# Kernel tuning notes

Measured on AMD Instinct MI355X. Metric: run time of the kernel, lower is better.

## Reference

```python
import jax, jax.numpy as jnp
import numpy as np

POOL = 2  # pool_size from init_kwargs


def setup_inputs() -> dict:
    key = jax.random.key(0)
    b, n = 8192, 64
    A = jax.random.normal(key, (b, n, n), dtype=jnp.float32)
    # SPD construction: A A^T / n + I  (well-conditioned, distinct eigvals a.s.)
    X = A @ jnp.swapaxes(A, -1, -2) / n + jnp.eye(n, dtype=jnp.float32)
    return {"X": X}


def _logm_spd(X):
    # matrix log of batched SPD via eigendecomposition (SPDTangentSpace)
    w, V = jnp.linalg.eigh(X)
    return (V * jnp.log(w)[..., None, :]) @ jnp.swapaxes(V, -1, -2)


def _expm_sym(H):
    # matrix exp of batched symmetric matrices (SPDUnTangentSpace)
    w, V = jnp.linalg.eigh(H)
    return (V * jnp.exp(w)[..., None, :]) @ jnp.swapaxes(V, -1, -2)


def reference(X):
    # log map to tangent space
    logX = _logm_spd(X)
    b, n, _ = logX.shape
    m = n // POOL
    # avg_pool2d(kernel=POOL, stride=POOL) over the (n, n) matrix dims
    pooled = logX.reshape(b, m, POOL, m, POOL).mean(axis=(2, 4))
    # pooling of a symmetric matrix with this block pattern stays symmetric;
    # symmetrize for numerical safety before eigh-based exp map
    pooled = 0.5 * (pooled + jnp.swapaxes(pooled, -1, -2))
    return _expm_sym(pooled)
```

## Files before the change

### kernel.cpp

```cpp
#include <hip/hip_runtime.h>

typedef __attribute__((ext_vector_type(8))) short short8;
typedef __attribute__((ext_vector_type(16))) float f32x16;

#define PL 8256
#define SLOT 16448
#define U0O 0
#define U1O SLOT
#define U2O (2 * SLOT)

__device__ __forceinline__ int swadr(int m, int kc) {
  return m * 128 + ((kc ^ (m & 7)) << 4);
}

__device__ __forceinline__ unsigned int cvtpk(float a, float b) {
  unsigned int r;
  asm("v_cvt_pk_bf16_f32 %0, %1, %2" : "=v"(r) : "v"(a), "v"(b));
  return r;
}

__device__ __forceinline__ float dppswap(float v) {
  return __int_as_float(
      __builtin_amdgcn_mov_dpp(__float_as_int(v), 0xB1, 0xF, 0xF, true));
}

__device__ __forceinline__ f32x16 zero16() {
  f32x16 z;
#pragma unroll
  for (int i = 0; i < 16; ++i) z[i] = 0.f;
  return z;
}

__device__ __forceinline__ void q16x16(f32x16& v) {
#pragma unroll
  for (int r = 0; r < 16; r += 2) {
    unsigned w = cvtpk(v[r], v[r + 1]);
    v[r] = __uint_as_float(w << 16);
    v[r + 1] = __uint_as_float(w & 0xFFFF0000u);
  }
}

__device__ __forceinline__ void store_hi8(char* dst, const float* v) {
  uint4 w = make_uint4(cvtpk(v[0], v[1]), cvtpk(v[2], v[3]),
                       cvtpk(v[4], v[5]), cvtpk(v[6], v[7]));
  *(uint4*)dst = w;
}

__device__ __forceinline__ void split_store8(char* dst, const float* v) {
  unsigned h[4], l[4];
#pragma unroll
  for (int j = 0; j < 4; ++j) {
    unsigned hw = cvtpk(v[2 * j], v[2 * j + 1]);
    float h0 = __uint_as_float(hw << 16);
    float h1 = __uint_as_float(hw & 0xFFFF0000u);
    l[j] = cvtpk(v[2 * j] - h0, v[2 * j + 1] - h1);
    h[j] = hw;
  }
  *(uint4*)dst = make_uint4(h[0], h[1], h[2], h[3]);
  *(uint4*)(dst + PL) = make_uint4(l[0], l[1], l[2], l[3]);
}

__device__ __forceinline__ void split_store4(char* dst, const float* v) {
  unsigned h0 = cvtpk(v[0], v[1]), h1 = cvtpk(v[2], v[3]);
  unsigned l0 = cvtpk(v[0] - __uint_as_float(h0 << 16),
                      v[1] - __uint_as_float(h0 & 0xFFFF0000u));
  unsigned l1 = cvtpk(v[2] - __uint_as_float(h1 << 16),
                      v[3] - __uint_as_float(h1 & 0xFFFF0000u));
  *(uint2*)dst = make_uint2(h0, h1);
  *(uint2*)(dst + PL) = make_uint2(l0, l1);
}

template <int NK, int OA, int OB>
__device__ __forceinline__ void mac1(f32x16& acc, char* const (&pA)[4],
                                     char* const (&pB)[4]) {
#pragma unroll
  for (int s = 0; s < NK; ++s) {
    short8 a = *(const short8*)(pA[s] + OA);
    short8 b = *(const short8*)(pB[s] + OB);
    acc = __builtin_amdgcn_mfma_f32_32x32x16_bf16(a, b, acc, 0, 0, 0);
  }
}

template <int NK, int OA, int OB>
__device__ __forceinline__ void mac2A(f32x16& acc, char* const (&pA)[4],
                                      char* const (&pB)[4]) {
#pragma unroll
  for (int s = 0; s < NK; ++s) {
    short8 ah = *(const short8*)(pA[s] + OA);
    short8 al = *(const short8*)(pA[s] + OA + PL);
    short8 b = *(const short8*)(pB[s] + OB);
    acc = __builtin_amdgcn_mfma_f32_32x32x16_bf16(ah, b, acc, 0, 0, 0);
    acc = __builtin_amdgcn_mfma_f32_32x32x16_bf16(al, b, acc, 0, 0, 0);
  }
}

template <int NK, int OA, int OB>
__device__ __forceinline__ void mac2B(f32x16& acc, char* const (&pA)[4],
                                      char* const (&pB)[4]) {
#pragma unroll
  for (int s = 0; s < NK; ++s) {
    short8 a = *(const short8*)(pA[s] + OA);
    short8 bh = *(const short8*)(pB[s] + OB);
    short8 bl = *(const short8*)(pB[s] + OB + PL);
    acc = __builtin_amdgcn_mfma_f32_32x32x16_bf16(a, bh, acc, 0, 0, 0);
    acc = __builtin_amdgcn_mfma_f32_32x32x16_bf16(a, bl, acc, 0, 0, 0);
  }
}

template <int NK, int OA, int OB>
__device__ __forceinline__ void mac3(f32x16& acc, char* const (&pA)[4],
                                     char* const (&pB)[4]) {
#pragma unroll
  for (int s = 0; s < NK; ++s) {
    short8 ah = *(const short8*)(pA[s] + OA);
    short8 al = *(const short8*)(pA[s] + OA + PL);
    short8 bh = *(const short8*)(pB[s] + OB);
    short8 bl = *(const short8*)(pB[s] + OB + PL);
    acc = __builtin_amdgcn_mfma_f32_32x32x16_bf16(ah, bh, acc, 0, 0, 0);
    acc = __builtin_amdgcn_mfma_f32_32x32x16_bf16(ah, bl, acc, 0, 0, 0);
    acc = __builtin_amdgcn_mfma_f32_32x32x16_bf16(al, bh, acc, 0, 0, 0);
  }
}

template <int OFF>
__device__ __forceinline__ void write_hi(char* lds, const int (&wo)[16], bool ev,
                                         const f32x16& vals) {
#pragma unroll
  for (int r = 0; r < 16; ++r) {
    float vn = dppswap(vals[r]);
    unsigned hw = cvtpk(vals[r], vn);
    if (ev) *(unsigned*)(lds + OFF + wo[r]) = hw;
  }
}

template <int OFF>
__device__ __forceinline__ void write_split(char* lds, const int (&wo)[16],
                                            bool ev, int pl, const f32x16& vals,
                                            int r0, int r1) {
#pragma unroll
  for (int r = 0; r < 16; ++r) {
    if (r < r0 || r >= r1) continue;
    float v = vals[r];
    float vn = dppswap(v);
    unsigned hw = cvtpk(v, vn);
    float lo = v - __uint_as_float(hw << 16);
    float lon = dppswap(lo);
    unsigned lw = cvtpk(lon, lo);
    *(unsigned*)(lds + OFF + pl + wo[r]) = ev ? hw : lw;
  }
}

__global__ void __launch_bounds__(256, 3)
spd_pool_kernel(const float* __restrict__ X, float* __restrict__ out) {
  __shared__ __align__(16) char lds[3 * SLOT];

  const int tid = threadIdx.x;
  const int lane = tid & 63;
  const int wv = tid >> 6;
  const int R = (wv >> 1) * 32;
  const int Cc = (wv & 1) * 32;
  const int half = lane >> 5;
  const int ln31 = lane & 31;
  const bool ev = (ln31 & 1) == 0;
  const int pl = ev ? 0 : PL;

  char* pA[4];
  char* pB[4];
#pragma unroll
  for (int s = 0; s < 4; ++s) {
    const int kc = 2 * s + half;
    pA[s] = lds + swadr(R + ln31, kc);
    pB[s] = lds + swadr(Cc + ln31, kc);
  }

  int wo[16];
  {
    const int col0 = Cc + (ln31 & ~1);
    const int cchunk = col0 >> 3, cbyte = (col0 & 7) * 2;
    const int rbase = R + 4 * half;
#pragma unroll
    for (int r = 0; r < 16; ++r) {
      const int m = rbase + (r & 3) + 8 * (r >> 2);
      wo[r] = m * 128 + ((cchunk ^ (m & 7)) << 4) + cbyte;
    }
  }

  f32x16 dmask;
#pragma unroll
  for (int r = 0; r < 16; ++r)
    dmask[r] = (R + (r & 3) + 8 * (r >> 2) + 4 * half == Cc + ln31) ? 1.f : 0.f;

  f32x16 mY, mZ;

  {
    const int em = tid >> 2;
    const int ekc = (tid & 3) * 2;
    const int ec0 = ekc * 8;
    const float ic1 = 1.0f / 6.6f;
    const float* Xg = X + (size_t)blockIdx.x * 4096 + em * 64 + ec0;
    const float4* xp = (const float4*)Xg;
    float4 a = xp[0], b = xp[1], c = xp[2], d = xp[3];
    float v[16] = {a.x * ic1, a.y * ic1, a.z * ic1, a.w * ic1,
                   b.x * ic1, b.y * ic1, b.z * ic1, b.w * ic1,
                   c.x * ic1, c.y * ic1, c.z * ic1, c.w * ic1,
                   d.x * ic1, d.y * ic1, d.z * ic1, d.w * ic1};
    float t[16];
#pragma unroll
    for (int i = 0; i < 16; ++i)
      t[i] = ((em == ec0 + i) ? 1.5f : 0.f) - 0.5f * v[i];
    split_store8(lds + swadr(em, ekc), v);
    split_store8(lds + swadr(em, ekc + 1), v + 8);
    store_hi8(lds + U1O + swadr(em, ekc), t);
    store_hi8(lds + U1O + swadr(em, ekc + 1), t + 8);
  }
  __syncthreads();
  mY = zero16();
  mac1<4, U0O, U1O>(mY, pA, pB);
  write_hi<U2O>(lds, wo, ev, mY);
  __syncthreads();
#pragma unroll 1
  for (int it = 0; it < 4; ++it) {
    f32x16 a;
#pragma unroll
    for (int r = 0; r < 16; ++r) a[r] = -3.f * dmask[r];
    mac1<4, U1O, U2O>(a, pA, pB);
    f32x16 tv;
#pragma unroll
    for (int r = 0; r < 16; ++r) tv[r] = -0.5f * a[r];
    write_hi<U2O + PL>(lds, wo, ev, tv);
    __syncthreads();
    mY = zero16();
    mac1<4, U2O, U2O + PL>(mY, pA, pB);
    mZ = zero16();
    mac1<4, U2O + PL, U1O>(mZ, pA, pB);
    __syncthreads();
    write_hi<U2O>(lds, wo, ev, mY);
    write_hi<U1O>(lds, wo, ev, mZ);
    __syncthreads();
  }
  mY = zero16();
  mac2A<4, U0O, U1O>(mY, pA, pB);
  write_split<U2O>(lds, wo, ev, pl, mY, 0, 16);
  __syncthreads();
  {
    f32x16 a;
#pragma unroll
    for (int r = 0; r < 16; ++r) a[r] = -dmask[r];
    mac2B<4, U1O, U2O>(a, pA, pB);
    f32x16 dv;
#pragma unroll
    for (int r = 0; r < 16; ++r) dv[r] = -0.5f * a[r];
    write_hi<U0O>(lds, wo, ev, dv);
  }
  __syncthreads();
  mac1<4, U2O, U0O>(mY, pA, pB);
  __syncthreads();
  write_split<U2O>(lds, wo, ev, pl, mY, 0, 16);
  {
    f32x16 t0v;
#pragma unroll
    for (int r = 0; r < 16; ++r) t0v[r] = 1.5f * dmask[r] - 0.5f * mY[r];
    write_hi<U1O>(lds, wo, ev, t0v);
  }
  __syncthreads();
  mY = zero16();
  mac1<4, U2O, U1O>(mY, pA, pB);
  write_hi<U0O>(lds, wo, ev, mY);
  __syncthreads();
#pragma unroll 1
  for (int it = 0; it < 2; ++it) {
    f32x16 a;
#pragma unroll
    for (int r = 0; r < 16; ++r) a[r] = -3.f * dmask[r];
    mac1<4, U1O, U0O>(a, pA, pB);
    f32x16 tv;
#pragma unroll
    for (int r = 0; r < 16; ++r) tv[r] = -0.5f * a[r];
    write_hi<U0O + PL>(lds, wo, ev, tv);
    __syncthreads();
    mY = zero16();
    mac1<4, U0O, U0O + PL>(mY, pA, pB);
    mZ = zero16();
    mac1<4, U0O + PL, U1O>(mZ, pA, pB);
    __syncthreads();
    write_hi<U0O>(lds, wo, ev, mY);
    write_hi<U1O>(lds, wo, ev, mZ);
    __syncthreads();
  }
  q16x16(mZ);
  mY = zero16();
  mac2A<4, U2O, U1O>(mY, pA, pB);
  write_split<U0O>(lds, wo, ev, pl, mY, 0, 16);
  __syncthreads();
  {
    f32x16 a;
#pragma unroll
    for (int r = 0; r < 16; ++r) a[r] = -dmask[r];
    mac2B<4, U1O, U0O>(a, pA, pB);
    f32x16 dv;
#pragma unroll
    for (int r = 0; r < 16; ++r) dv[r] = -0.5f * a[r];
    write_hi<U2O>(lds, wo, ev, dv);
  }
  __syncthreads();
  mac1<4, U0O, U2O>(mY, pA, pB);
  mac1<4, U2O, U1O>(mZ, pA, pB);
  __syncthreads();
  write_split<U0O>(lds, wo, ev, pl, mY, 0, 16);
  q16x16(mZ);
  write_hi<U1O>(lds, wo, ev, mZ);
  __syncthreads();
  {
    f32x16 a;
#pragma unroll
    for (int r = 0; r < 16; ++r) a[r] = -dmask[r];
    mac2B<4, U1O, U0O>(a, pA, pB);
    f32x16 dv;
#pragma unroll
    for (int r = 0; r < 16; ++r) dv[r] = -0.5f * a[r];
    write_hi<U2O>(lds, wo, ev, dv);
  }
  __syncthreads();
  mac1<4, U0O, U2O>(mY, pA, pB);
  mac1<4, U2O, U1O>(mZ, pA, pB);
  f32x16 sv;
  {
    const float ca = 0.80141224f;
    const float cb = 0.31194493f;
#pragma unroll
    for (int r = 0; r < 16; ++r) sv[r] = ca * mY[r] - cb * mZ[r];
  }
  __syncthreads();
  write_split<U0O>(lds, wo, ev, pl, sv, 0, 16);
  __syncthreads();
  {
    f32x16 s2 = zero16();
    mac3<4, U0O, U0O>(s2, pA, pB);
    const float A11 = -0.08948864f, A9 = 0.12152778f;
    f32x16 qv;
#pragma unroll
    for (int r = 0; r < 16; ++r) qv[r] = A11 * s2[r] + A9 * dmask[r];
    write_hi<U1O>(lds, wo, ev, s2);
    write_hi<U1O + PL>(lds, wo, ev, qv);
  }
  __syncthreads();
  {
    const float acoef[3] = {-0.17857143f, 0.3f, -0.66666667f};
#pragma unroll 1
    for (int j = 0; j < 3; ++j) {
      f32x16 a;
#pragma unroll
      for (int r = 0; r < 16; ++r) a[r] = acoef[j] * dmask[r];
      mac1<4, U1O + PL, U1O>(a, pA, pB);
      __syncthreads();
      write_hi<U1O + PL>(lds, wo, ev, a);
      __syncthreads();
    }
  }
  {
    f32x16 a;
#pragma unroll
    for (int r = 0; r < 16; ++r) a[r] = 4.f * dmask[r];
    mac1<4, U1O + PL, U1O>(a, pA, pB);
    __syncthreads();
    write_split<U2O>(lds, wo, ev, pl, a, 0, 16);
    __syncthreads();
  }
  {
    f32x16 mL = zero16();
    mac3<4, U0O, U2O>(mL, pA, pB);
    float* Lf = (float*)(lds + U1O);
#pragma unroll
    for (int r = 0; r < 16; ++r)
      Lf[(R + (r & 3) + 8 * (r >> 2) + 4 * half) * 64 + Cc + ln31] = mL[r];
  }
  __syncthreads();
  {
    const float d8 = 2.4801587e-5f, d7 = 1.9841270e-4f;
    const float* Lf = (const float*)(lds + U1O);
    int i = tid >> 3, ct = tid & 7, j4 = ct * 4;
    const float4* r0p = (const float4*)&Lf[(2 * i) * 64 + 8 * ct];
    const float4* r1p = (const float4*)&Lf[(2 * i + 1) * 64 + 8 * ct];
    float4 a0 = r0p[0], a1 = r0p[1], b0 = r1p[0], b1 = r1p[1];
    float p[4], q2v[4];
    p[0] = 0.125f * (a0.x + a0.y + b0.x + b0.y);
    p[1] = 0.125f * (a0.z + a0.w + b0.z + b0.w);
    p[2] = 0.125f * (a1.x + a1.y + b1.x + b1.y);
    p[3] = 0.125f * (a1.z + a1.w + b1.z + b1.w);
#pragma unroll
    for (int qq = 0; qq < 4; ++qq)
      q2v[qq] = d8 * p[qq] + ((i == j4 + qq) ? d7 : 0.f);
    int boff = swadr(i, ct >> 1) + (j4 & 7) * 2;
    split_store4(lds + boff, p);
    split_store4(lds + U2O + boff, q2v);
  }
  __syncthreads();
  char* pE[4];
#pragma unroll
  for (int s = 0; s < 4; ++s) pE[s] = lds + swadr(ln31, 2 * s + half);
  f32x16 dmask2;
#pragma unroll
  for (int r = 0; r < 16; ++r)
    dmask2[r] = ((r & 3) + 8 * (r >> 2) + 4 * half == ln31) ? 1.f : 0.f;
  int wo2[16];
  {
    const int col0 = ln31 & ~1;
    const int cchunk = col0 >> 3, cbyte = (col0 & 7) * 2;
    const int rbase = 4 * half;
#pragma unroll
    for (int r = 0; r < 16; ++r) {
      const int m = rbase + (r & 3) + 8 * (r >> 2);
      wo2[r] = m * 128 + ((cchunk ^ (m & 7)) << 4) + cbyte;
    }
  }
  {
    const float dcoef[7] = {1.f / 720.f, 1.f / 120.f, 1.f / 24.f,
                            1.f / 6.f,   0.5f,        1.f,       1.f};
#pragma unroll 1
    for (int j = 0; j < 7; ++j) {
      f32x16 acc;
#pragma unroll
      for (int r = 0; r < 16; ++r) acc[r] = dcoef[j] * dmask2[r];
      mac3<2, U2O, U0O>(acc, pE, pE);
      __syncthreads();
      write_split<U2O>(lds, wo2, ev, pl, acc, 4 * wv, 4 * wv + 4);
      __syncthreads();
    }
  }
  {
    f32x16 acc = zero16();
    mac3<2, U2O, U2O>(acc, pE, pE);
    float* og = out + (size_t)blockIdx.x * 1024;
#pragma unroll
    for (int r = 0; r < 16; ++r) {
      if (r < 4 * wv || r >= 4 * wv + 4) continue;
      int rl = (r & 3) + 8 * (r >> 2) + 4 * half;
      og[rl * 32 + ln31] = acc[r];
    }
  }
}

extern "C" void kernel_launch(void* const* d_in, const int* in_sizes, int n_in,
                              void* d_out, int out_size, void* d_ws, size_t ws_size,
                              hipStream_t stream) {
  const float* X = (const float*)d_in[0];
  float* out = (float*)d_out;
  const int batch = in_sizes[0] / 4096;
  spd_pool_kernel<<<batch, 256, 0, stream>>>(X, out);
}
```

Before: 541.5 us.

## Shrink LDS to five 8KB planes and pool in registers via DPP

Shared memory is reorganised from three padded 16448-byte slots into five unpadded 8KB planes (40KB instead of about 48KB), and launch bounds go from 3 to 4 blocks per CU so more workgroups can be resident. The 2x2 average pooling no longer stages the fp32 log matrix through LDS with an extra barrier. It is now computed in registers from the MFMA accumulator, using a DPP lane swap for the column pair. The results are split into bf16 hi/lo and written directly into the planes. The risks are register pressure under the tighter launch bound, more LDS bank conflicts now that the padding is gone, and many narrow 2-byte stores.

```diff
diff --git a/kernel.cpp b/kernel.cpp
--- a/kernel.cpp
+++ b/kernel.cpp
@@ -3,11 +3,12 @@
 typedef __attribute__((ext_vector_type(8))) short short8;
 typedef __attribute__((ext_vector_type(16))) float f32x16;
 
-#define PL 8256
-#define SLOT 16448
-#define U0O 0
-#define U1O SLOT
-#define U2O (2 * SLOT)
+#define PL 8192
+#define PP0 0
+#define PP1 8192
+#define PP2 16384
+#define PP3 24576
+#define PP4 32768
 
 __device__ __forceinline__ int swadr(int m, int kc) {
   return m * 128 + ((kc ^ (m & 7)) << 4);
@@ -18,19 +19,16 @@
   asm("v_cvt_pk_bf16_f32 %0, %1, %2" : "=v"(r) : "v"(a), "v"(b));
   return r;
 }
-
 __device__ __forceinline__ float dppswap(float v) {
   return __int_as_float(
       __builtin_amdgcn_mov_dpp(__float_as_int(v), 0xB1, 0xF, 0xF, true));
 }
-
 __device__ __forceinline__ f32x16 zero16() {
   f32x16 z;
 #pragma unroll
   for (int i = 0; i < 16; ++i) z[i] = 0.f;
   return z;
 }
-
 __device__ __forceinline__ void q16x16(f32x16& v) {
 #pragma unroll
   for (int r = 0; r < 16; r += 2) {
@@ -41,11 +39,9 @@
 }
 
 __device__ __forceinline__ void store_hi8(char* dst, const float* v) {
-  uint4 w = make_uint4(cvtpk(v[0], v[1]), cvtpk(v[2], v[3]),
-                       cvtpk(v[4], v[5]), cvtpk(v[6], v[7]));
-  *(uint4*)dst = w;
-}
-
+  *(uint4*)dst = make_uint4(cvtpk(v[0], v[1]), cvtpk(v[2], v[3]),
+                            cvtpk(v[4], v[5]), cvtpk(v[6], v[7]));
+}
 __device__ __forceinline__ void split_store8(char* dst, const float* v) {
   unsigned h[4], l[4];
 #pragma unroll
@@ -60,19 +56,9 @@
   *(uint4*)(dst + PL) = make_uint4(l[0], l[1], l[2], l[3]);
 }
 
-__device__ __forceinline__ void split_store4(char* dst, const float* v) {
-  unsigned h0 = cvtpk(v[0], v[1]), h1 = cvtpk(v[2], v[3]);
-  unsigned l0 = cvtpk(v[0] - __uint_as_float(h0 << 16),
-                      v[1] - __uint_as_float(h0 & 0xFFFF0000u));
-  unsigned l1 = cvtpk(v[2] - __uint_as_float(h1 << 16),
-                      v[3] - __uint_as_float(h1 & 0xFFFF0000u));
-  *(uint2*)dst = make_uint2(h0, h1);
-  *(uint2*)(dst + PL) = make_uint2(l0, l1);
-}
-
-template <int NK, int OA, int OB>
-__device__ __forceinline__ void mac1(f32x16& acc, char* const (&pA)[4],
-                                     char* const (&pB)[4]) {
+template <int NK, int OA, int OB, int N>
+__device__ __forceinline__ void mac1(f32x16& acc, char* const (&pA)[N],
+                                     char* const (&pB)[N]) {
 #pragma unroll
   for (int s = 0; s < NK; ++s) {
     short8 a = *(const short8*)(pA[s] + OA);
@@ -80,10 +66,9 @@
     acc = __builtin_amdgcn_mfma_f32_32x32x16_bf16(a, b, acc, 0, 0, 0);
   }
 }
-
-template <int NK, int OA, int OB>
-__device__ __forceinline__ void mac2A(f32x16& acc, char* const (&pA)[4],
-                                      char* const (&pB)[4]) {
+template <int NK, int OA, int OB, int N>
+__device__ __forceinline__ void mac2A(f32x16& acc, char* const (&pA)[N],
+                                      char* const (&pB)[N]) {
 #pragma unroll
   for (int s = 0; s < NK; ++s) {
     short8 ah = *(const short8*)(pA[s] + OA);
@@ -93,10 +78,9 @@
     acc = __builtin_amdgcn_mfma_f32_32x32x16_bf16(al, b, acc, 0, 0, 0);
   }
 }
-
-template <int NK, int OA, int OB>
-__device__ __forceinline__ void mac2B(f32x16& acc, char* const (&pA)[4],
-                                      char* const (&pB)[4]) {
+template <int NK, int OA, int OB, int N>
+__device__ __forceinline__ void mac2B(f32x16& acc, char* const (&pA)[N],
+                                      char* const (&pB)[N]) {
 #pragma unroll
   for (int s = 0; s < NK; ++s) {
     short8 a = *(const short8*)(pA[s] + OA);
@@ -106,10 +90,9 @@
     acc = __builtin_amdgcn_mfma_f32_32x32x16_bf16(a, bl, acc, 0, 0, 0);
   }
 }
-
-template <int NK, int OA, int OB>
-__device__ __forceinline__ void mac3(f32x16& acc, char* const (&pA)[4],
-                                     char* const (&pB)[4]) {
+template <int NK, int OA, int OB, int N>
+__device__ __forceinline__ void mac3(f32x16& acc, char* const (&pA)[N],
+                                     char* const (&pB)[N]) {
 #pragma unroll
   for (int s = 0; s < NK; ++s) {
     short8 ah = *(const short8*)(pA[s] + OA);
@@ -132,7 +115,6 @@
     if (ev) *(unsigned*)(lds + OFF + wo[r]) = hw;
   }
 }
-
 template <int OFF>
 __device__ __forceinline__ void write_split(char* lds, const int (&wo)[16],
                                             bool ev, int pl, const f32x16& vals,
@@ -150,9 +132,9 @@
   }
 }
 
-__global__ void __launch_bounds__(256, 3)
+__global__ void __launch_bounds__(256, 4)
 spd_pool_kernel(const float* __restrict__ X, float* __restrict__ out) {
-  __shared__ __align__(16) char lds[3 * SLOT];
+  __shared__ __align__(16) char lds[5 * 8192];
 
   const int tid = threadIdx.x;
   const int lane = tid & 63;
@@ -172,7 +154,6 @@
     pA[s] = lds + swadr(R + ln31, kc);
     pB[s] = lds + swadr(Cc + ln31, kc);
   }
-
   int wo[16];
   {
     const int col0 = Cc + (ln31 & ~1);
@@ -184,7 +165,6 @@
       wo[r] = m * 128 + ((cchunk ^ (m & 7)) << 4) + cbyte;
     }
   }
-
   f32x16 dmask;
 #pragma unroll
   for (int r = 0; r < 16; ++r)
@@ -208,121 +188,121 @@
 #pragma unroll
     for (int i = 0; i < 16; ++i)
       t[i] = ((em == ec0 + i) ? 1.5f : 0.f) - 0.5f * v[i];
-    split_store8(lds + swadr(em, ekc), v);
-    split_store8(lds + swadr(em, ekc + 1), v + 8);
-    store_hi8(lds + U1O + swadr(em, ekc), t);
-    store_hi8(lds + U1O + swadr(em, ekc + 1), t + 8);
+    split_store8(lds + PP0 + swadr(em, ekc), v);
+    split_store8(lds + PP0 + swadr(em, ekc + 1), v + 8);
+    store_hi8(lds + PP2 + swadr(em, ekc), t);
+    store_hi8(lds + PP2 + swadr(em, ekc + 1), t + 8);
   }
   __syncthreads();
   mY = zero16();
-  mac1<4, U0O, U1O>(mY, pA, pB);
-  write_hi<U2O>(lds, wo, ev, mY);
+  mac1<4, PP0, PP2>(mY, pA, pB);
+  write_hi<PP3>(lds, wo, ev, mY);
   __syncthreads();
 #pragma unroll 1
   for (int it = 0; it < 4; ++it) {
     f32x16 a;
 #pragma unroll
     for (int r = 0; r < 16; ++r) a[r] = -3.f * dmask[r];
-    mac1<4, U1O, U2O>(a, pA, pB);
+    mac1<4, PP2, PP3>(a, pA, pB);
     f32x16 tv;
 #pragma unroll
     for (int r = 0; r < 16; ++r) tv[r] = -0.5f * a[r];
-    write_hi<U2O + PL>(lds, wo, ev, tv);
+    write_hi<PP4>(lds, wo, ev, tv);
     __syncthreads();
     mY = zero16();
-    mac1<4, U2O, U2O + PL>(mY, pA, pB);
+    mac1<4, PP3, PP4>(mY, pA, pB);
     mZ = zero16();
-    mac1<4, U2O + PL, U1O>(mZ, pA, pB);
-    __syncthreads();
-    write_hi<U2O>(lds, wo, ev, mY);
-    write_hi<U1O>(lds, wo, ev, mZ);
+    mac1<4, PP4, PP2>(mZ, pA, pB);
+    __syncthreads();
+    write_hi<PP3>(lds, wo, ev, mY);
+    write_hi<PP2>(lds, wo, ev, mZ);
     __syncthreads();
   }
   mY = zero16();
-  mac2A<4, U0O, U1O>(mY, pA, pB);
-  write_split<U2O>(lds, wo, ev, pl, mY, 0, 16);
+  mac2A<4, PP0, PP2>(mY, pA, pB);
+  write_split<PP3>(lds, wo, ev, pl, mY, 0, 16);
   __syncthreads();
   {
     f32x16 a;
 #pragma unroll
     for (int r = 0; r < 16; ++r) a[r] = -dmask[r];
-    mac2B<4, U1O, U2O>(a, pA, pB);
+    mac2B<4, PP2, PP3>(a, pA, pB);
     f32x16 dv;
 #pragma unroll
     for (int r = 0; r < 16; ++r) dv[r] = -0.5f * a[r];
-    write_hi<U0O>(lds, wo, ev, dv);
-  }
-  __syncthreads();
-  mac1<4, U2O, U0O>(mY, pA, pB);
-  __syncthreads();
-  write_split<U2O>(lds, wo, ev, pl, mY, 0, 16);
+    write_hi<PP0>(lds, wo, ev, dv);
+  }
+  __syncthreads();
+  mac1<4, PP3, PP0>(mY, pA, pB);
+  __syncthreads();
+  write_split<PP3>(lds, wo, ev, pl, mY, 0, 16);
   {
     f32x16 t0v;
 #pragma unroll
     for (int r = 0; r < 16; ++r) t0v[r] = 1.5f * dmask[r] - 0.5f * mY[r];
-    write_hi<U1O>(lds, wo, ev, t0v);
+    write_hi<PP2>(lds, wo, ev, t0v);
   }
   __syncthreads();
   mY = zero16();
-  mac1<4, U2O, U1O>(mY, pA, pB);
-  write_hi<U0O>(lds, wo, ev, mY);
+  mac1<4, PP3, PP2>(mY, pA, pB);
+  write_hi<PP0>(lds, wo, ev, mY);
   __syncthreads();
 #pragma unroll 1
   for (int it = 0; it < 2; ++it) {
     f32x16 a;
 #pragma unroll
     for (int r = 0; r < 16; ++r) a[r] = -3.f * dmask[r];
-    mac1<4, U1O, U0O>(a, pA, pB);
+    mac1<4, PP2, PP0>(a, pA, pB);
     f32x16 tv;
 #pragma unroll
     for (int r = 0; r < 16; ++r) tv[r] = -0.5f * a[r];
-    write_hi<U0O + PL>(lds, wo, ev, tv);
+    write_hi<PP1>(lds, wo, ev, tv);
     __syncthreads();
     mY = zero16();
-    mac1<4, U0O, U0O + PL>(mY, pA, pB);
+    mac1<4, PP0, PP1>(mY, pA, pB);
     mZ = zero16();
-    mac1<4, U0O + PL, U1O>(mZ, pA, pB);
-    __syncthreads();
-    write_hi<U0O>(lds, wo, ev, mY);
-    write_hi<U1O>(lds, wo, ev, mZ);
+    mac1<4, PP1, PP2>(mZ, pA, pB);
+    __syncthreads();
+    write_hi<PP0>(lds, wo, ev, mY);
+    write_hi<PP2>(lds, wo, ev, mZ);
     __syncthreads();
   }
   q16x16(mZ);
   mY = zero16();
-  mac2A<4, U2O, U1O>(mY, pA, pB);
-  write_split<U0O>(lds, wo, ev, pl, mY, 0, 16);
+  mac2A<4, PP3, PP2>(mY, pA, pB);
+  write_split<PP0>(lds, wo, ev, pl, mY, 0, 16);
   __syncthreads();
   {
     f32x16 a;
 #pragma unroll
     for (int r = 0; r < 16; ++r) a[r] = -dmask[r];
-    mac2B<4, U1O, U0O>(a, pA, pB);
+    mac2B<4, PP2, PP0>(a, pA, pB);
     f32x16 dv;
 #pragma unroll
     for (int r = 0; r < 16; ++r) dv[r] = -0.5f * a[r];
-    write_hi<U2O>(lds, wo, ev, dv);
-  }
-  __syncthreads();
-  mac1<4, U0O, U2O>(mY, pA, pB);
-  mac1<4, U2O, U1O>(mZ, pA, pB);
-  __syncthreads();
-  write_split<U0O>(lds, wo, ev, pl, mY, 0, 16);
+    write_hi<PP3>(lds, wo, ev, dv);
+  }
+  __syncthreads();
+  mac1<4, PP0, PP3>(mY, pA, pB);
+  mac1<4, PP3, PP2>(mZ, pA, pB);
+  __syncthreads();
+  write_split<PP0>(lds, wo, ev, pl, mY, 0, 16);
   q16x16(mZ);
-  write_hi<U1O>(lds, wo, ev, mZ);
+  write_hi<PP2>(lds, wo, ev, mZ);
   __syncthreads();
   {
     f32x16 a;
 #pragma unroll
     for (int r = 0; r < 16; ++r) a[r] = -dmask[r];
-    mac2B<4, U1O, U0O>(a, pA, pB);
+    mac2B<4, PP2, PP0>(a, pA, pB);
     f32x16 dv;
 #pragma unroll
     for (int r = 0; r < 16; ++r) dv[r] = -0.5f * a[r];
-    write_hi<U2O>(lds, wo, ev, dv);
-  }
-  __syncthreads();
-  mac1<4, U0O, U2O>(mY, pA, pB);
-  mac1<4, U2O, U1O>(mZ, pA, pB);
+    write_hi<PP3>(lds, wo, ev, dv);
+  }
+  __syncthreads();
+  mac1<4, PP0, PP3>(mY, pA, pB);
+  mac1<4, PP3, PP2>(mZ, pA, pB);
   f32x16 sv;
   {
     const float ca = 0.80141224f;
@@ -331,17 +311,17 @@
     for (int r = 0; r < 16; ++r) sv[r] = ca * mY[r] - cb * mZ[r];
   }
   __syncthreads();
-  write_split<U0O>(lds, wo, ev, pl, sv, 0, 16);
+  write_split<PP0>(lds, wo, ev, pl, sv, 0, 16);
   __syncthreads();
   {
     f32x16 s2 = zero16();
-    mac3<4, U0O, U0O>(s2, pA, pB);
+    mac3<4, PP0, PP0>(s2, pA, pB);
     const float A11 = -0.08948864f, A9 = 0.12152778f;
     f32x16 qv;
 #pragma unroll
     for (int r = 0; r < 16; ++r) qv[r] = A11 * s2[r] + A9 * dmask[r];
-    write_hi<U1O>(lds, wo, ev, s2);
-    write_hi<U1O + PL>(lds, wo, ev, qv);
+    write_hi<PP2>(lds, wo, ev, s2);
+    write_hi<PP3>(lds, wo, ev, qv);
   }
   __syncthreads();
   {
@@ -351,9 +331,9 @@
       f32x16 a;
 #pragma unroll
       for (int r = 0; r < 16; ++r) a[r] = acoef[j] * dmask[r];
-      mac1<4, U1O + PL, U1O>(a, pA, pB);
+      mac1<4, PP3, PP2>(a, pA, pB);
       __syncthreads();
-      write_hi<U1O + PL>(lds, wo, ev, a);
+      write_hi<PP3>(lds, wo, ev, a);
       __syncthreads();
     }
   }
@@ -361,43 +341,43 @@
     f32x16 a;
 #pragma unroll
     for (int r = 0; r < 16; ++r) a[r] = 4.f * dmask[r];
-    mac1<4, U1O + PL, U1O>(a, pA, pB);
-    __syncthreads();
-    write_split<U2O>(lds, wo, ev, pl, a, 0, 16);
+    mac1<4, PP3, PP2>(a, pA, pB);
+    __syncthreads();
+    write_split<PP3>(lds, wo, ev, pl, a, 0, 16);
     __syncthreads();
   }
   {
     f32x16 mL = zero16();
-    mac3<4, U0O, U2O>(mL, pA, pB);
-    float* Lf = (float*)(lds + U1O);
-#pragma unroll
-    for (int r = 0; r < 16; ++r)
-      Lf[(R + (r & 3) + 8 * (r >> 2) + 4 * half) * 64 + Cc + ln31] = mL[r];
-  }
-  __syncthreads();
-  {
+    mac3<4, PP0, PP3>(mL, pA, pB);
+    __syncthreads();
     const float d8 = 2.4801587e-5f, d7 = 1.9841270e-4f;
-    const float* Lf = (const float*)(lds + U1O);
-    int i = tid >> 3, ct = tid & 7, j4 = ct * 4;
-    const float4* r0p = (const float4*)&Lf[(2 * i) * 64 + 8 * ct];
-    const float4* r1p = (const float4*)&Lf[(2 * i + 1) * 64 + 8 * ct];
-    float4 a0 = r0p[0], a1 = r0p[1], b0 = r1p[0], b1 = r1p[1];
-    float p[4], q2v[4];
-    p[0] = 0.125f * (a0.x + a0.y + b0.x + b0.y);
-    p[1] = 0.125f * (a0.z + a0.w + b0.z + b0.w);
-    p[2] = 0.125f * (a1.x + a1.y + b1.x + b1.y);
-    p[3] = 0.125f * (a1.z + a1.w + b1.z + b1.w);
-#pragma unroll
-    for (int qq = 0; qq < 4; ++qq)
-      q2v[qq] = d8 * p[qq] + ((i == j4 + qq) ? d7 : 0.f);
-    int boff = swadr(i, ct >> 1) + (j4 & 7) * 2;
-    split_store4(lds + boff, p);
-    split_store4(lds + U2O + boff, q2v);
-  }
-  __syncthreads();
-  char* pE[4];
-#pragma unroll
-  for (int s = 0; s < 4; ++s) pE[s] = lds + swadr(ln31, 2 * s + half);
+#pragma unroll
+    for (int q = 0; q < 8; ++q) {
+      float rp = mL[2 * q] + mL[2 * q + 1];
+      float cs = rp + dppswap(rp);
+      float p = 0.125f * cs;
+      const int row = R / 2 + (q & 1) + 4 * (q >> 1) + 2 * half;
+      const int col = Cc / 2 + (ln31 >> 1);
+      float qv = d8 * p + ((row == col) ? d7 : 0.f);
+      unsigned phw = cvtpk(p, p);
+      float plo = p - __uint_as_float(phw << 16);
+      unsigned plw = cvtpk(plo, plo);
+      unsigned qhw = cvtpk(qv, qv);
+      float qlo = qv - __uint_as_float(qhw << 16);
+      unsigned qlw = cvtpk(qlo, qlo);
+      const int off = row * 128 + (((col >> 3) ^ (row & 7)) << 4) + (col & 7) * 2;
+      if (ev) {
+        *(short*)(lds + PP0 + off) = (short)phw;
+        *(short*)(lds + PP1 + off) = (short)plw;
+        *(short*)(lds + PP2 + off) = (short)qhw;
+        *(short*)(lds + PP3 + off) = (short)qlw;
+      }
+    }
+  }
+  __syncthreads();
+  char* pE[2];
+#pragma unroll
+  for (int s = 0; s < 2; ++s) pE[s] = lds + swadr(ln31, 2 * s + half);
   f32x16 dmask2;
 #pragma unroll
   for (int r = 0; r < 16; ++r)
@@ -421,15 +401,15 @@
       f32x16 acc;
 #pragma unroll
       for (int r = 0; r < 16; ++r) acc[r] = dcoef[j] * dmask2[r];
-      mac3<2, U2O, U0O>(acc, pE, pE);
+      mac3<2, PP2, PP0>(acc, pE, pE);
       __syncthreads();
-      write_split<U2O>(lds, wo2, ev, pl, acc, 4 * wv, 4 * wv + 4);
+      write_split<PP2>(lds, wo2, ev, pl, acc, 4 * wv, 4 * wv + 4);
       __syncthreads();
     }
   }
   {
     f32x16 acc = zero16();
-    mac3<2, U2O, U2O>(acc, pE, pE);
+    mac3<2, PP2, PP2>(acc, pE, pE);
     float* og = out + (size_t)blockIdx.x * 1024;
 #pragma unroll
     for (int r = 0; r < 16; ++r) {
```

New measurement: 491.6 us. 9.2% less time.
